# Performance work log

Measured on AMD Instinct MI355X. Metric: run time of the kernel, lower is better.

Reference implementation:

```python
import jax, jax.numpy as jnp
import numpy as np
import math

H = 8
D_MODEL = 4096
D_K = D_MODEL // H  # 512; Sk must equal D_K for the im_attn @ value matmul
B, SQ, SK = 4, 2048, 512


def _linear_params(key, fan_in, fan_out):
    kw, kb = jax.random.split(key)
    bound = 1.0 / math.sqrt(fan_in)
    W = jax.random.uniform(kw, (fan_out, fan_in), jnp.float32, -bound, bound)
    b = jax.random.uniform(kb, (fan_out,), jnp.float32, -bound, bound)
    return W, b


def setup_inputs() -> dict:
    key = jax.random.key(0)
    ks = jax.random.split(key, 8)
    query = jax.random.normal(ks[0], (B, SQ, D_MODEL), jnp.float32)
    k_in = jax.random.normal(ks[1], (B, SK, D_MODEL), jnp.float32)
    v_in = jax.random.normal(ks[2], (B, SK, D_MODEL), jnp.float32)
    image_feat = jax.random.normal(ks[3], (B, SK, D_MODEL), jnp.float32)
    W0, b0 = _linear_params(ks[4], D_MODEL, D_MODEL)
    W1, b1 = _linear_params(ks[5], D_MODEL, D_MODEL)
    W2, b2 = _linear_params(ks[6], D_MODEL, D_MODEL)
    W3, b3 = _linear_params(ks[7], D_MODEL, D_MODEL)  # reused for image_feat AND output proj (as in source)
    return {"query": query, "key": k_in, "value": v_in, "image_feat": image_feat,
            "W0": W0, "b0": b0, "W1": W1, "b1": b1, "W2": W2, "b2": b2, "W3": W3, "b3": b3}


def _split_heads(x):
    # [b, s, d_model] -> [b, h, s, d_k]
    b, s, _ = x.shape
    return x.reshape(b, s, H, D_K).transpose(0, 2, 1, 3)


def reference(query, key, value, image_feat, W0, b0, W1, b1, W2, b2, W3, b3):
    q = _split_heads(query @ W0.T + b0)        # [b,h,Sq,d_k]
    k = _split_heads(key @ W1.T + b1)          # [b,h,Sk,d_k]
    v = _split_heads(value @ W2.T + b2)        # [b,h,Sk,d_k]
    imf = _split_heads(image_feat @ W3.T + b3) # [b,h,Sk,d_k]

    scores = jnp.einsum('bhqd,bhkd->bhqk', q, k) / math.sqrt(D_K)  # [b,h,Sq,Sk]
    p_attn = jax.nn.softmax(scores, axis=-1)
    # second-stage attention over feature axis (Sk == d_k so shapes line up)
    im_attn = jax.nn.softmax(jnp.einsum('bhqk,bhkd->bhqd', p_attn, imf), axis=-1)  # [b,h,Sq,d_k]
    x = jnp.einsum('bhqs,bhsd->bhqd', im_attn, v)  # contracts d_k axis of im_attn with Sk axis of v

    x = x.transpose(0, 2, 1, 3).reshape(query.shape[0], -1, H * D_K)  # [b,Sq,d_model]
    return x @ W3.T + b3  # linears[-1] is the same (shared) 4th linear
```

## Files before the change

### kernel.cpp

```cpp
#include <hip/hip_runtime.h>
#include <hip/hip_bf16.h>
#include <stdint.h>

#define B_   4
#define H_   8
#define SQ_  2048
#define SK_  512
#define DM_  4096
#define DK_  512

typedef __bf16 bf16;
typedef __bf16 bf16x8 __attribute__((ext_vector_type(8)));
typedef float  fx4    __attribute__((ext_vector_type(4)));

typedef __attribute__((address_space(1))) void gv_t;
typedef __attribute__((address_space(3))) void lv_t;

__global__ void sniff_dtype(const uint32_t* __restrict__ q, int* __restrict__ flag)
{
    const int l = threadIdx.x;
    int cnt = 0;
    #pragma unroll
    for (int i = 0; i < 4; ++i) {
        const uint32_t u = q[l * 4 + i];
        const int e = (u >> 7) & 0xFF;
        cnt += (e >= 100 && e <= 135) ? 1 : 0;
    }
    #pragma unroll
    for (int s = 1; s < 64; s <<= 1) cnt += __shfl_xor(cnt, s);
    if (l == 0) *flag = (cnt < 150) ? 1 : 0;
}

__global__ __launch_bounds__(256) void cvt_to_bf16(
    const void* __restrict__ in, bf16* __restrict__ out, const int* __restrict__ flagp)
{
    const size_t i = ((size_t)blockIdx.x * 256 + threadIdx.x) * 8;
    if (*flagp) {
        const float4* p = (const float4*)((const float*)in + i);
        const float4 u0 = p[0], u1 = p[1];
        bf16x8 v;
        v[0] = (bf16)u0.x; v[1] = (bf16)u0.y; v[2] = (bf16)u0.z; v[3] = (bf16)u0.w;
        v[4] = (bf16)u1.x; v[5] = (bf16)u1.y; v[6] = (bf16)u1.z; v[7] = (bf16)u1.w;
        *(bf16x8*)(out + i) = v;
    } else {
        *(bf16x8*)(out + i) = *(const bf16x8*)((const bf16*)in + i);
    }
}

__global__ __launch_bounds__(256, 3) void gemm_bt(
    const bf16* __restrict__ A, const bf16* __restrict__ Bt,
    void* __restrict__ Cv, const void* __restrict__ biasv,
    int K, int lda, int ldb, int ldc, float alpha,
    long long sAb, long long sAh, long long sBb, long long sBh,
    long long sCb, long long sCh,
    const int* __restrict__ flagp, int ebits)
{
    __shared__ bf16 sA[128 * 64];
    __shared__ bf16 sB[128 * 64];

    const int fl = ebits ? *flagp : 0;
    const bool bias32 = fl && (ebits & 1);
    const bool c32    = fl && (ebits & 2);

    const int z = blockIdx.z;
    const int bz = z >> 3, hz = z & 7;
    const bf16* Ab = A  + (size_t)bz * sAb + (size_t)hz * sAh;
    const bf16* Bb = Bt + (size_t)bz * sBb + (size_t)hz * sBh;
    const size_t offC = (size_t)bz * sCb + (size_t)hz * sCh;

    const int n0 = blockIdx.x * 128;
    const int m0 = blockIdx.y * 128;

    const int t = threadIdx.x;
    const int w = t >> 6, l = t & 63;
    const int lrow = l >> 3, lcol = l & 7;
    const int wm = (w >> 1) * 64, wn = (w & 1) * 64;
    const int ml = l & 15, quad = l >> 4;

    const bf16* pa[4];
    const bf16* pb[4];
    #pragma unroll
    for (int i = 0; i < 4; ++i) {
        const int c = w * 4 + i;
        const int r = c * 8 + lrow;
        const int jj = lcol ^ (r & 7);
        pa[i] = Ab + (size_t)(m0 + r) * lda + jj * 8;
        pb[i] = Bb + (size_t)(n0 + r) * ldb + jj * 8;
    }

    fx4 acc[4][4];
    const fx4 zero = {0.f, 0.f, 0.f, 0.f};
    #pragma unroll
    for (int i = 0; i < 4; ++i)
        #pragma unroll
        for (int j = 0; j < 4; ++j) acc[i][j] = zero;

    for (int kt = 0; kt < K; kt += 64) {
        #pragma unroll
        for (int i = 0; i < 4; ++i) {
            const int c = w * 4 + i;
            __builtin_amdgcn_global_load_lds((gv_t*)(pa[i] + kt), (lv_t*)(sA + c * 512), 16, 0, 0);
            __builtin_amdgcn_global_load_lds((gv_t*)(pb[i] + kt), (lv_t*)(sB + c * 512), 16, 0, 0);
        }
        __syncthreads();

        #pragma unroll
        for (int kk = 0; kk < 64; kk += 32) {
            bf16x8 af[4], bfr[4];
            const int jbase = (kk >> 3) + quad;
            #pragma unroll
            for (int mi = 0; mi < 4; ++mi) {
                const int r = wm + mi * 16 + ml;
                af[mi] = *(const bf16x8*)&sA[r * 64 + ((jbase ^ (r & 7)) << 3)];
            }
            #pragma unroll
            for (int ni = 0; ni < 4; ++ni) {
                const int r = wn + ni * 16 + ml;
                bfr[ni] = *(const bf16x8*)&sB[r * 64 + ((jbase ^ (r & 7)) << 3)];
            }
            #pragma unroll
            for (int mi = 0; mi < 4; ++mi)
                #pragma unroll
                for (int ni = 0; ni < 4; ++ni)
                    acc[mi][ni] = __builtin_amdgcn_mfma_f32_16x16x32_bf16(
                        af[mi], bfr[ni], acc[mi][ni], 0, 0, 0);
        }
        __syncthreads();
    }

    #pragma unroll
    for (int ni = 0; ni < 4; ++ni) {
        const int cg = n0 + wn + ni * 16 + ml;
        const float bv = biasv ? (bias32 ? ((const float*)biasv)[cg] : (float)((const bf16*)biasv)[cg]) : 0.f;
        #pragma unroll
        for (int mi = 0; mi < 4; ++mi) {
            const int rg = m0 + wm + mi * 16 + quad * 4;
            #pragma unroll
            for (int r = 0; r < 4; ++r) {
                const float val = acc[mi][ni][r] * alpha + bv;
                const size_t idx = offC + (size_t)(rg + r) * ldc + cg;
                if (c32) ((float*)Cv)[idx] = val;
                else     ((bf16*)Cv)[idx] = (bf16)val;
            }
        }
    }
}

#define ISSUE_TILE(tt, bb)                                                        \
    do {                                                                          \
        _Pragma("unroll")                                                         \
        for (int i_ = 0; i_ < 4; ++i_) {                                          \
            const int c_ = w * 4 + i_;                                            \
            __builtin_amdgcn_global_load_lds((gv_t*)(pa[i_] + (size_t)(tt) * 64), \
                (lv_t*)(&sm[bb][0][c_ * 512]), 16, 0, 0);                         \
            __builtin_amdgcn_global_load_lds((gv_t*)(pb[i_] + (size_t)(tt) * 64), \
                (lv_t*)(&sm[bb][1][c_ * 512]), 16, 0, 0);                         \
        }                                                                         \
    } while (0)

#define LDS_FRAG(dst, base, fr, kI)                                               \
    dst = *(const bf16x8*)&base[(fr) * 64 + ((((kI) * 4 + quad) ^ ((fr) & 7)) << 3)]

__global__ __launch_bounds__(512, 2) void gemm256(
    const bf16* __restrict__ A, const bf16* __restrict__ Bt,
    void* __restrict__ Cv, const void* __restrict__ biasv,
    int K, int lda, int ldb, int ldc, float alpha,
    long long sAb, long long sAh, long long sBb, long long sBh,
    long long sCb, long long sCh,
    const int* __restrict__ flagp, int ebits)
{
    __shared__ bf16 sm[2][2][256 * 64];

    const int fl = ebits ? *flagp : 0;
    const bool bias32 = fl && (ebits & 1);
    const bool c32    = fl && (ebits & 2);

    const int gX = gridDim.x, gY = gridDim.y;
    int idx = (blockIdx.z * gY + blockIdx.y) * gX + blockIdx.x;
    const int nwg = gX * gY * gridDim.z;
    if ((nwg & 7) == 0) idx = (idx & 7) * (nwg >> 3) + (idx >> 3);
    const int bx = idx % gX;
    const int tmpi = idx / gX;
    const int by = tmpi % gY;
    const int z  = tmpi / gY;

    const int bz = z >> 3, hz = z & 7;
    const bf16* Ab = A  + (size_t)bz * sAb + (size_t)hz * sAh;
    const bf16* Bb = Bt + (size_t)bz * sBb + (size_t)hz * sBh;
    const size_t offC = (size_t)bz * sCb + (size_t)hz * sCh;

    const int n0 = bx * 256;
    const int m0 = by * 256;

    const int t  = threadIdx.x;
    const int w  = t >> 6, l = t & 63;
    const int lrow = l >> 3, lcol = l & 7;
    const int wr = w >> 2, wc = w & 3;
    const int R0 = wr * 128, C0 = wc * 64;
    const int ml = l & 15, quad = l >> 4;

    const bf16* pa[4];
    const bf16* pb[4];
    #pragma unroll
    for (int i = 0; i < 4; ++i) {
        const int c = w * 4 + i;
        const int r = c * 8 + lrow;
        const int jj = lcol ^ (r & 7);
        pa[i] = Ab + (size_t)(m0 + r) * lda + jj * 8;
        pb[i] = Bb + (size_t)(n0 + r) * ldb + jj * 8;
    }

    fx4 acc[8][4];
    const fx4 zero = {0.f, 0.f, 0.f, 0.f};
    #pragma unroll
    for (int i = 0; i < 8; ++i)
        #pragma unroll
        for (int j = 0; j < 4; ++j) acc[i][j] = zero;

    const int nt = K >> 6;

    ISSUE_TILE(0, 0);
    ISSUE_TILE(1, 1);
    asm volatile("s_waitcnt vmcnt(8)" ::: "memory");
    asm volatile("s_barrier" ::: "memory");

    for (int tt = 0; tt < nt; ++tt) {
        const int b = tt & 1;
        const bf16* sA = sm[b][0];
        const bf16* sB = sm[b][1];

        bf16x8 af[4][2];
        bf16x8 b0f[2][2];
        bf16x8 b1f[2][2];

        #pragma unroll
        for (int im = 0; im < 4; ++im)
            #pragma unroll
            for (int kI = 0; kI < 2; ++kI)
                LDS_FRAG(af[im][kI], sA, R0 + im * 16 + ml, kI);
        #pragma unroll
        for (int in = 0; in < 2; ++in)
            #pragma unroll
            for (int kI = 0; kI < 2; ++kI)
                LDS_FRAG(b0f[in][kI], sB, C0 + in * 16 + ml, kI);
        asm volatile("s_barrier" ::: "memory");

        __builtin_amdgcn_s_setprio(1);
        #pragma unroll
        for (int kI = 0; kI < 2; ++kI)
            #pragma unroll
            for (int im = 0; im < 4; ++im)
                #pragma unroll
                for (int in = 0; in < 2; ++in)
                    acc[im][in] = __builtin_amdgcn_mfma_f32_16x16x32_bf16(
                        af[im][kI], b0f[in][kI], acc[im][in], 0, 0, 0);
        __builtin_amdgcn_s_setprio(0);
        #pragma unroll
        for (int in = 0; in < 2; ++in)
            #pragma unroll
            for (int kI = 0; kI < 2; ++kI)
                LDS_FRAG(b1f[in][kI], sB, C0 + 32 + in * 16 + ml, kI);
        asm volatile("s_barrier" ::: "memory");

        __builtin_amdgcn_s_setprio(1);
        #pragma unroll
        for (int kI = 0; kI < 2; ++kI)
            #pragma unroll
            for (int im = 0; im < 4; ++im)
                #pragma unroll
                for (int in = 0; in < 2; ++in)
                    acc[im][2 + in] = __builtin_amdgcn_mfma_f32_16x16x32_bf16(
                        af[im][kI], b1f[in][kI], acc[im][2 + in], 0, 0, 0);
        __builtin_amdgcn_s_setprio(0);
        #pragma unroll
        for (int im = 0; im < 4; ++im)
            #pragma unroll
            for (int kI = 0; kI < 2; ++kI)
                LDS_FRAG(af[im][kI], sA, R0 + 64 + im * 16 + ml, kI);
        asm volatile("s_barrier" ::: "memory");

        __builtin_amdgcn_s_setprio(1);
        #pragma unroll
        for (int kI = 0; kI < 2; ++kI)
            #pragma unroll
            for (int im = 0; im < 4; ++im)
                #pragma unroll
                for (int in = 0; in < 2; ++in)
                    acc[4 + im][2 + in] = __builtin_amdgcn_mfma_f32_16x16x32_bf16(
                        af[im][kI], b1f[in][kI], acc[4 + im][2 + in], 0, 0, 0);
        __builtin_amdgcn_s_setprio(0);
        asm volatile("s_barrier" ::: "memory");

        __builtin_amdgcn_s_setprio(1);
        #pragma unroll
        for (int kI = 0; kI < 2; ++kI)
            #pragma unroll
            for (int im = 0; im < 4; ++im)
                #pragma unroll
                for (int in = 0; in < 2; ++in)
                    acc[4 + im][in] = __builtin_amdgcn_mfma_f32_16x16x32_bf16(
                        af[im][kI], b0f[in][kI], acc[4 + im][in], 0, 0, 0);
        __builtin_amdgcn_s_setprio(0);

        if (tt + 1 >= nt) break;
        if (tt + 2 < nt) {
            ISSUE_TILE(tt + 2, b);
            asm volatile("s_waitcnt vmcnt(8)" ::: "memory");
        } else {
            asm volatile("s_waitcnt vmcnt(0)" ::: "memory");
        }
        asm volatile("s_barrier" ::: "memory");
    }

    #pragma unroll
    for (int ni = 0; ni < 4; ++ni) {
        const int cg = n0 + C0 + ni * 16 + ml;
        const float bv = biasv ? (bias32 ? ((const float*)biasv)[cg] : (float)((const bf16*)biasv)[cg]) : 0.f;
        #pragma unroll
        for (int mi = 0; mi < 8; ++mi) {
            const int rg = m0 + R0 + mi * 16 + quad * 4;
            #pragma unroll
            for (int r = 0; r < 4; ++r) {
                const float val = acc[mi][ni][r] * alpha + bv;
                const size_t idx = offC + (size_t)(rg + r) * ldc + cg;
                if (c32) ((float*)Cv)[idx] = val;
                else     ((bf16*)Cv)[idx] = (bf16)val;
            }
        }
    }
}

__global__ __launch_bounds__(256) void softmax512(bf16* __restrict__ buf)
{
    const int row = blockIdx.x * 4 + (threadIdx.x >> 6);
    const int l = threadIdx.x & 63;
    bf16* p = buf + (size_t)row * 512 + l * 8;
    bf16x8 v = *(const bf16x8*)p;
    float f[8];
    float mx = -1e30f;
    #pragma unroll
    for (int j = 0; j < 8; ++j) {
        f[j] = (float)v[j];
        if (!(fabsf(f[j]) < 1e30f)) f[j] = -1e9f;
        mx = fmaxf(mx, f[j]);
    }
    #pragma unroll
    for (int s = 1; s < 64; s <<= 1) mx = fmaxf(mx, __shfl_xor(mx, s));
    float sum = 0.f;
    #pragma unroll
    for (int j = 0; j < 8; ++j) { f[j] = __expf(f[j] - mx); sum += f[j]; }
    #pragma unroll
    for (int s = 1; s < 64; s <<= 1) sum += __shfl_xor(sum, s);
    const float inv = 1.f / sum;
    #pragma unroll
    for (int j = 0; j < 8; ++j) v[j] = (bf16)(f[j] * inv);
    *(bf16x8*)p = v;
}

__global__ __launch_bounds__(256) void transpose_heads(
    const bf16* __restrict__ in, bf16* __restrict__ out)
{
    __shared__ bf16 tile[32][33];
    const int z = blockIdx.z, b = z >> 3, h = z & 7;
    const int s0 = blockIdx.x * 32, d0 = blockIdx.y * 32;
    const int tx = threadIdx.x, ty = threadIdx.y;
    #pragma unroll
    for (int j = 0; j < 4; ++j) {
        const int s = s0 + ty + j * 8;
        tile[ty + j * 8][tx] = in[(size_t)b * SK_ * DM_ + (size_t)s * DM_ + h * DK_ + d0 + tx];
    }
    __syncthreads();
    #pragma unroll
    for (int j = 0; j < 4; ++j) {
        const int d = d0 + ty + j * 8;
        out[(size_t)z * DK_ * SK_ + (size_t)d * SK_ + s0 + tx] = tile[tx][ty + j * 8];
    }
}

extern "C" void kernel_launch(void* const* d_in, const int* in_sizes, int n_in,
                              void* d_out, int out_size, void* d_ws, size_t ws_size,
                              hipStream_t stream)
{
    const void* query = d_in[0];
    const void* key   = d_in[1];
    const void* value = d_in[2];
    const void* imf   = d_in[3];
    const void* W0 = d_in[4];  const void* b0 = d_in[5];
    const void* W1 = d_in[6];  const void* b1 = d_in[7];
    const void* W2 = d_in[8];  const void* b2 = d_in[9];
    const void* W3 = d_in[10]; const void* b3 = d_in[11];

    bf16* ws    = (bf16*)d_ws;
    int*  flagp = (int*)d_ws;
    bf16* wslot = ws + 8;
    bf16* R     = ws + 8 + 16777216;
    bf16* inbuf = R;
    bf16* vproj = R + 8388608;
    bf16* imfp  = R + 16777216;
    bf16* s1    = R;
    bf16* xcat  = R;

    bf16* obase = (bf16*)d_out;
    bf16* qproj = obase;
    bf16* qbf   = obase + 33554432;
    bf16* kproj = obase + 33554432;
    bf16* vT    = obase + 41943040;
    bf16* imfT  = obase + 50331648;
    bf16* s2    = obase;

    const float inv_sqrt_dk = 0.04419417382415922f;

    sniff_dtype<<<1, 64, 0, stream>>>((const uint32_t*)query, flagp);

    cvt_to_bf16<<<16384, 256, 0, stream>>>(query, qbf, flagp);
    cvt_to_bf16<<<8192, 256, 0, stream>>>(W0, wslot, flagp);
    gemm256<<<dim3(16, 32, 1), 512, 0, stream>>>(qbf, wslot, qproj, b0,
        4096, 4096, 4096, 4096, 1.f, 0,0,0,0,0,0, flagp, 1);
    cvt_to_bf16<<<4096, 256, 0, stream>>>(key, inbuf, flagp);
    cvt_to_bf16<<<8192, 256, 0, stream>>>(W1, wslot, flagp);
    gemm_bt<<<dim3(32, 16, 1), 256, 0, stream>>>(inbuf, wslot, kproj, b1,
        4096, 4096, 4096, 4096, 1.f, 0,0,0,0,0,0, flagp, 1);
    cvt_to_bf16<<<4096, 256, 0, stream>>>(value, inbuf, flagp);
    cvt_to_bf16<<<8192, 256, 0, stream>>>(W2, wslot, flagp);
    gemm_bt<<<dim3(32, 16, 1), 256, 0, stream>>>(inbuf, wslot, vproj, b2,
        4096, 4096, 4096, 4096, 1.f, 0,0,0,0,0,0, flagp, 1);
    cvt_to_bf16<<<4096, 256, 0, stream>>>(imf, inbuf, flagp);
    cvt_to_bf16<<<8192, 256, 0, stream>>>(W3, wslot, flagp);
    gemm_bt<<<dim3(32, 16, 1), 256, 0, stream>>>(inbuf, wslot, imfp, b3,
        4096, 4096, 4096, 4096, 1.f, 0,0,0,0,0,0, flagp, 1);

    transpose_heads<<<dim3(16, 16, 32), dim3(32, 8), 0, stream>>>(vproj, vT);
    transpose_heads<<<dim3(16, 16, 32), dim3(32, 8), 0, stream>>>(imfp, imfT);

    gemm256<<<dim3(2, 8, 32), 512, 0, stream>>>(qproj, kproj, s1, nullptr,
        512, 4096, 4096, 512, inv_sqrt_dk,
        (long long)SQ_*DM_, (long long)DK_, (long long)SK_*DM_, (long long)DK_,
        (long long)H_*SQ_*SK_, (long long)SQ_*SK_, flagp, 0);
    softmax512<<<dim3(16384), 256, 0, stream>>>(s1);
    gemm256<<<dim3(2, 8, 32), 512, 0, stream>>>(s1, imfT, s2, nullptr,
        512, 512, 512, 512, 1.f,
        (long long)H_*SQ_*SK_, (long long)SQ_*SK_, (long long)H_*DK_*SK_, (long long)DK_*SK_,
        (long long)H_*SQ_*SK_, (long long)SQ_*SK_, flagp, 0);
    softmax512<<<dim3(16384), 256, 0, stream>>>(s2);
    gemm256<<<dim3(2, 8, 32), 512, 0, stream>>>(s2, vT, xcat, nullptr,
        512, 512, 512, 4096, 1.f,
        (long long)H_*SQ_*SK_, (long long)SQ_*SK_, (long long)H_*DK_*SK_, (long long)DK_*SK_,
        (long long)SQ_*DM_, (long long)DK_, flagp, 0);
    cvt_to_bf16<<<8192, 256, 0, stream>>>(W3, wslot, flagp);
    gemm256<<<dim3(16, 32, 1), 512, 0, stream>>>(xcat, wslot, d_out, b3,
        4096, 4096, 4096, 4096, 1.f, 0,0,0,0,0,0, flagp, 3);
}
```

Before: 1.605 ms.

## Software-pipeline LDS fragment loads across K tiles and drop intra-tile barriers

Restructures the GEMM main loop so the A and B0 fragments for the next K tile are read from shared memory during the last MFMA quadrants of the current tile. Three of the four per-tile barriers are removed, leaving one barrier per iteration after the global prefetch issue. The aim is to hide LDS read latency behind MFMA work and cut synchronisation stalls. The cost is extra fragment registers (aN, aP, b0N), which may raise VGPR pressure, and a reordering that has to stay correct with respect to the buffer being overwritten by the next global load.

After: 1.617 ms. No clear change (+0.8%).

```diff
diff --git a/kernel.cpp b/kernel.cpp
--- a/kernel.cpp
+++ b/kernel.cpp
@@ -219,31 +219,30 @@
 
     const int nt = K >> 6;
 
+    bf16x8 aN[4][2], aP[4][2], b0N[2][2], b1f[2][2];
+
     ISSUE_TILE(0, 0);
     ISSUE_TILE(1, 1);
     asm volatile("s_waitcnt vmcnt(8)" ::: "memory");
     asm volatile("s_barrier" ::: "memory");
+    #pragma unroll
+    for (int im = 0; im < 4; ++im)
+        #pragma unroll
+        for (int kI = 0; kI < 2; ++kI)
+            LDS_FRAG(aN[im][kI], (&sm[0][0][0]), R0 + im * 16 + ml, kI);
+    #pragma unroll
+    for (int in = 0; in < 2; ++in)
+        #pragma unroll
+        for (int kI = 0; kI < 2; ++kI)
+            LDS_FRAG(b0N[in][kI], (&sm[0][1][0]), C0 + in * 16 + ml, kI);
 
     for (int tt = 0; tt < nt; ++tt) {
         const int b = tt & 1;
-        const bf16* sA = sm[b][0];
-        const bf16* sB = sm[b][1];
-
-        bf16x8 af[4][2];
-        bf16x8 b0f[2][2];
-        bf16x8 b1f[2][2];
-
-        #pragma unroll
-        for (int im = 0; im < 4; ++im)
-            #pragma unroll
-            for (int kI = 0; kI < 2; ++kI)
-                LDS_FRAG(af[im][kI], sA, R0 + im * 16 + ml, kI);
-        #pragma unroll
-        for (int in = 0; in < 2; ++in)
-            #pragma unroll
-            for (int kI = 0; kI < 2; ++kI)
-                LDS_FRAG(b0f[in][kI], sB, C0 + in * 16 + ml, kI);
-        asm volatile("s_barrier" ::: "memory");
+        const bf16* sA  = sm[b][0];
+        const bf16* sB  = sm[b][1];
+        const bf16* sAn = sm[b ^ 1][0];
+        const bf16* sBn = sm[b ^ 1][1];
+        const bool more = (tt + 1 < nt);
 
         __builtin_amdgcn_s_setprio(1);
         #pragma unroll
@@ -253,14 +252,13 @@
                 #pragma unroll
                 for (int in = 0; in < 2; ++in)
                     acc[im][in] = __builtin_amdgcn_mfma_f32_16x16x32_bf16(
-                        af[im][kI], b0f[in][kI], acc[im][in], 0, 0, 0);
+                        aN[im][kI], b0N[in][kI], acc[im][in], 0, 0, 0);
         __builtin_amdgcn_s_setprio(0);
         #pragma unroll
         for (int in = 0; in < 2; ++in)
             #pragma unroll
             for (int kI = 0; kI < 2; ++kI)
                 LDS_FRAG(b1f[in][kI], sB, C0 + 32 + in * 16 + ml, kI);
-        asm volatile("s_barrier" ::: "memory");
 
         __builtin_amdgcn_s_setprio(1);
         #pragma unroll
@@ -270,39 +268,15 @@
                 #pragma unroll
                 for (int in = 0; in < 2; ++in)
                     acc[im][2 + in] = __builtin_amdgcn_mfma_f32_16x16x32_bf16(
-                        af[im][kI], b1f[in][kI], acc[im][2 + in], 0, 0, 0);
+                        aN[im][kI], b1f[in][kI], acc[im][2 + in], 0, 0, 0);
         __builtin_amdgcn_s_setprio(0);
         #pragma unroll
         for (int im = 0; im < 4; ++im)
             #pragma unroll
             for (int kI = 0; kI < 2; ++kI)
-                LDS_FRAG(af[im][kI], sA, R0 + 64 + im * 16 + ml, kI);
+                LDS_FRAG(aP[im][kI], sA, R0 + 64 + im * 16 + ml, kI);
+
         asm volatile("s_barrier" ::: "memory");
-
-        __builtin_amdgcn_s_setprio(1);
-        #pragma unroll
-        for (int kI = 0; kI < 2; ++kI)
-            #pragma unroll
-            for (int im = 0; im < 4; ++im)
-                #pragma unroll
-                for (int in = 0; in < 2; ++in)
-                    acc[4 + im][2 + in] = __builtin_amdgcn_mfma_f32_16x16x32_bf16(
-                        af[im][kI], b1f[in][kI], acc[4 + im][2 + in], 0, 0, 0);
-        __builtin_amdgcn_s_setprio(0);
-        asm volatile("s_barrier" ::: "memory");
-
-        __builtin_amdgcn_s_setprio(1);
-        #pragma unroll
-        for (int kI = 0; kI < 2; ++kI)
-            #pragma unroll
-            for (int im = 0; im < 4; ++im)
-                #pragma unroll
-                for (int in = 0; in < 2; ++in)
-                    acc[4 + im][in] = __builtin_amdgcn_mfma_f32_16x16x32_bf16(
-                        af[im][kI], b0f[in][kI], acc[4 + im][in], 0, 0, 0);
-        __builtin_amdgcn_s_setprio(0);
-
-        if (tt + 1 >= nt) break;
         if (tt + 2 < nt) {
             ISSUE_TILE(tt + 2, b);
             asm volatile("s_waitcnt vmcnt(8)" ::: "memory");
@@ -310,6 +284,42 @@
             asm volatile("s_waitcnt vmcnt(0)" ::: "memory");
         }
         asm volatile("s_barrier" ::: "memory");
+
+        __builtin_amdgcn_s_setprio(1);
+        #pragma unroll
+        for (int kI = 0; kI < 2; ++kI)
+            #pragma unroll
+            for (int im = 0; im < 4; ++im)
+                #pragma unroll
+                for (int in = 0; in < 2; ++in)
+                    acc[4 + im][2 + in] = __builtin_amdgcn_mfma_f32_16x16x32_bf16(
+                        aP[im][kI], b1f[in][kI], acc[4 + im][2 + in], 0, 0, 0);
+        __builtin_amdgcn_s_setprio(0);
+        if (more) {
+            #pragma unroll
+            for (int im = 0; im < 4; ++im)
+                #pragma unroll
+                for (int kI = 0; kI < 2; ++kI)
+                    LDS_FRAG(aN[im][kI], sAn, R0 + im * 16 + ml, kI);
+        }
+
+        __builtin_amdgcn_s_setprio(1);
+        #pragma unroll
+        for (int kI = 0; kI < 2; ++kI)
+            #pragma unroll
+            for (int im = 0; im < 4; ++im)
+                #pragma unroll
+                for (int in = 0; in < 2; ++in)
+                    acc[4 + im][in] = __builtin_amdgcn_mfma_f32_16x16x32_bf16(
+                        aP[im][kI], b0N[in][kI], acc[4 + im][in], 0, 0, 0);
+        __builtin_amdgcn_s_setprio(0);
+        if (more) {
+            #pragma unroll
+            for (int in = 0; in < 2; ++in)
+                #pragma unroll
+                for (int kI = 0; kI < 2; ++kI)
+                    LDS_FRAG(b0N[in][kI], sBn, C0 + in * 16 + ml, kI);
+        }
     }
 
     #pragma unroll
```

## Replace 256x256 GEMM with 256x128 tile, BK=32 pipelined kernel

Applied to the files above, without the earlier changes.

Replaces the 512-thread 256x256 tile, BK=64 GEMM with a 256-thread kernel using 256x128 output tiles and 32-wide K slices. It adopts a new XOR swizzle and collapses the four barrier-separated MFMA phases into two. The tile loads for the next stage are issued mid-iteration so they overlap the remaining MFMAs. The aim is fewer barriers per unit of work and more workgroups to fill the CUs. In exchange, operand reuse per block drops, global traffic per FLOP rises, and each K-step carries more loop overhead.

Result: slower. 1.715 ms (+6.8%).

```diff
diff --git a/kernel.cpp b/kernel.cpp
--- a/kernel.cpp
+++ b/kernel.cpp
@@ -146,22 +146,24 @@
     }
 }
 
-#define ISSUE_TILE(tt, bb)                                                        \
-    do {                                                                          \
-        _Pragma("unroll")                                                         \
-        for (int i_ = 0; i_ < 4; ++i_) {                                          \
-            const int c_ = w * 4 + i_;                                            \
-            __builtin_amdgcn_global_load_lds((gv_t*)(pa[i_] + (size_t)(tt) * 64), \
-                (lv_t*)(&sm[bb][0][c_ * 512]), 16, 0, 0);                         \
-            __builtin_amdgcn_global_load_lds((gv_t*)(pb[i_] + (size_t)(tt) * 64), \
-                (lv_t*)(&sm[bb][1][c_ * 512]), 16, 0, 0);                         \
-        }                                                                         \
+#define ISSUE_TILE6(tt, bb)                                                         \
+    do {                                                                            \
+        bf16* bufA_ = sm + (bb) * 12288;                                            \
+        bf16* bufB_ = bufA_ + 8192;                                                 \
+        _Pragma("unroll")                                                           \
+        for (int i_ = 0; i_ < 4; ++i_)                                              \
+            __builtin_amdgcn_global_load_lds((gv_t*)(pa[i_] + (size_t)(tt) * 32),   \
+                (lv_t*)(bufA_ + (w * 4 + i_) * 512), 16, 0, 0);                     \
+        _Pragma("unroll")                                                           \
+        for (int i_ = 0; i_ < 2; ++i_)                                              \
+            __builtin_amdgcn_global_load_lds((gv_t*)(pb[i_] + (size_t)(tt) * 32),   \
+                (lv_t*)(bufB_ + (w * 2 + i_) * 512), 16, 0, 0);                     \
     } while (0)
 
-#define LDS_FRAG(dst, base, fr, kI)                                               \
-    dst = *(const bf16x8*)&base[(fr) * 64 + ((((kI) * 4 + quad) ^ ((fr) & 7)) << 3)]
-
-__global__ __launch_bounds__(512, 2) void gemm256(
+#define LDS_FRAG32(dst, base, fr)                                                   \
+    dst = *(const bf16x8*)&base[(fr) * 32 + (((quad ^ (((fr) >> 1) & 3))) << 3)]
+
+__global__ __launch_bounds__(256, 2) void gemm_pipe(
     const bf16* __restrict__ A, const bf16* __restrict__ Bt,
     void* __restrict__ Cv, const void* __restrict__ biasv,
     int K, int lda, int ldb, int ldc, float alpha,
@@ -169,7 +171,7 @@
     long long sCb, long long sCh,
     const int* __restrict__ flagp, int ebits)
 {
-    __shared__ bf16 sm[2][2][256 * 64];
+    __shared__ bf16 sm[2 * 12288];
 
     const int fl = ebits ? *flagp : 0;
     const bool bias32 = fl && (ebits & 1);
@@ -189,24 +191,28 @@
     const bf16* Bb = Bt + (size_t)bz * sBb + (size_t)hz * sBh;
     const size_t offC = (size_t)bz * sCb + (size_t)hz * sCh;
 
-    const int n0 = bx * 256;
+    const int n0 = bx * 128;
     const int m0 = by * 256;
 
     const int t  = threadIdx.x;
     const int w  = t >> 6, l = t & 63;
-    const int lrow = l >> 3, lcol = l & 7;
-    const int wr = w >> 2, wc = w & 3;
+    const int wr = w >> 1, wc = w & 1;
     const int R0 = wr * 128, C0 = wc * 64;
     const int ml = l & 15, quad = l >> 4;
 
+    const int srow = l >> 2, sslot = l & 3;
     const bf16* pa[4];
-    const bf16* pb[4];
+    const bf16* pb[2];
     #pragma unroll
     for (int i = 0; i < 4; ++i) {
-        const int c = w * 4 + i;
-        const int r = c * 8 + lrow;
-        const int jj = lcol ^ (r & 7);
+        const int r = (w * 4 + i) * 16 + srow;
+        const int jj = sslot ^ ((r >> 1) & 3);
         pa[i] = Ab + (size_t)(m0 + r) * lda + jj * 8;
+    }
+    #pragma unroll
+    for (int i = 0; i < 2; ++i) {
+        const int r = (w * 2 + i) * 16 + srow;
+        const int jj = sslot ^ ((r >> 1) & 3);
         pb[i] = Bb + (size_t)(n0 + r) * ldb + jj * 8;
     }
 
@@ -217,99 +223,77 @@
         #pragma unroll
         for (int j = 0; j < 4; ++j) acc[i][j] = zero;
 
-    const int nt = K >> 6;
-
-    ISSUE_TILE(0, 0);
-    ISSUE_TILE(1, 1);
-    asm volatile("s_waitcnt vmcnt(8)" ::: "memory");
+    const int nt = K >> 5;
+
+    ISSUE_TILE6(0, 0);
+    ISSUE_TILE6(1, 1);
+    asm volatile("s_waitcnt vmcnt(6)" ::: "memory");
     asm volatile("s_barrier" ::: "memory");
 
     for (int tt = 0; tt < nt; ++tt) {
         const int b = tt & 1;
-        const bf16* sA = sm[b][0];
-        const bf16* sB = sm[b][1];
-
-        bf16x8 af[4][2];
-        bf16x8 b0f[2][2];
-        bf16x8 b1f[2][2];
-
-        #pragma unroll
-        for (int im = 0; im < 4; ++im)
-            #pragma unroll
-            for (int kI = 0; kI < 2; ++kI)
-                LDS_FRAG(af[im][kI], sA, R0 + im * 16 + ml, kI);
+        const bf16* sA = sm + b * 12288;
+        const bf16* sB = sA + 8192;
+
+        bf16x8 aF[4], b0[2], b1[2];
+
+        #pragma unroll
+        for (int im = 0; im < 4; ++im)
+            LDS_FRAG32(aF[im], sA, R0 + im * 16 + ml);
         #pragma unroll
         for (int in = 0; in < 2; ++in)
-            #pragma unroll
-            for (int kI = 0; kI < 2; ++kI)
-                LDS_FRAG(b0f[in][kI], sB, C0 + in * 16 + ml, kI);
+            LDS_FRAG32(b0[in], sB, C0 + in * 16 + ml);
+
+        __builtin_amdgcn_s_setprio(1);
+        #pragma unroll
+        for (int im = 0; im < 4; ++im)
+            #pragma unroll
+            for (int in = 0; in < 2; ++in)
+                acc[im][in] = __builtin_amdgcn_mfma_f32_16x16x32_bf16(
+                    aF[im], b0[in], acc[im][in], 0, 0, 0);
+        __builtin_amdgcn_s_setprio(0);
+        #pragma unroll
+        for (int in = 0; in < 2; ++in)
+            LDS_FRAG32(b1[in], sB, C0 + 32 + in * 16 + ml);
+
+        __builtin_amdgcn_s_setprio(1);
+        #pragma unroll
+        for (int im = 0; im < 4; ++im)
+            #pragma unroll
+            for (int in = 0; in < 2; ++in)
+                acc[im][2 + in] = __builtin_amdgcn_mfma_f32_16x16x32_bf16(
+                    aF[im], b1[in], acc[im][2 + in], 0, 0, 0);
+        __builtin_amdgcn_s_setprio(0);
+        #pragma unroll
+        for (int im = 0; im < 4; ++im)
+            LDS_FRAG32(aF[im], sA, R0 + 64 + im * 16 + ml);
+
         asm volatile("s_barrier" ::: "memory");
-
-        __builtin_amdgcn_s_setprio(1);
-        #pragma unroll
-        for (int kI = 0; kI < 2; ++kI)
-            #pragma unroll
-            for (int im = 0; im < 4; ++im)
-                #pragma unroll
-                for (int in = 0; in < 2; ++in)
-                    acc[im][in] = __builtin_amdgcn_mfma_f32_16x16x32_bf16(
-                        af[im][kI], b0f[in][kI], acc[im][in], 0, 0, 0);
-        __builtin_amdgcn_s_setprio(0);
-        #pragma unroll
-        for (int in = 0; in < 2; ++in)
-            #pragma unroll
-            for (int kI = 0; kI < 2; ++kI)
-                LDS_FRAG(b1f[in][kI], sB, C0 + 32 + in * 16 + ml, kI);
-        asm volatile("s_barrier" ::: "memory");
-
-        __builtin_amdgcn_s_setprio(1);
-        #pragma unroll
-        for (int kI = 0; kI < 2; ++kI)
-            #pragma unroll
-            for (int im = 0; im < 4; ++im)
-                #pragma unroll
-                for (int in = 0; in < 2; ++in)
-                    acc[im][2 + in] = __builtin_amdgcn_mfma_f32_16x16x32_bf16(
-                        af[im][kI], b1f[in][kI], acc[im][2 + in], 0, 0, 0);
-        __builtin_amdgcn_s_setprio(0);
-        #pragma unroll
-        for (int im = 0; im < 4; ++im)
-            #pragma unroll
-            for (int kI = 0; kI < 2; ++kI)
-                LDS_FRAG(af[im][kI], sA, R0 + 64 + im * 16 + ml, kI);
-        asm volatile("s_barrier" ::: "memory");
-
-        __builtin_amdgcn_s_setprio(1);
-        #pragma unroll
-        for (int kI = 0; kI < 2; ++kI)
-            #pragma unroll
-            for (int im = 0; im < 4; ++im)
-                #pragma unroll
-                for (int in = 0; in < 2; ++in)
-                    acc[4 + im][2 + in] = __builtin_amdgcn_mfma_f32_16x16x32_bf16(
-                        af[im][kI], b1f[in][kI], acc[4 + im][2 + in], 0, 0, 0);
-        __builtin_amdgcn_s_setprio(0);
-        asm volatile("s_barrier" ::: "memory");
-
-        __builtin_amdgcn_s_setprio(1);
-        #pragma unroll
-        for (int kI = 0; kI < 2; ++kI)
-            #pragma unroll
-            for (int im = 0; im < 4; ++im)
-                #pragma unroll
-                for (int in = 0; in < 2; ++in)
-                    acc[4 + im][in] = __builtin_amdgcn_mfma_f32_16x16x32_bf16(
-                        af[im][kI], b0f[in][kI], acc[4 + im][in], 0, 0, 0);
-        __builtin_amdgcn_s_setprio(0);
-
-        if (tt + 1 >= nt) break;
         if (tt + 2 < nt) {
-            ISSUE_TILE(tt + 2, b);
-            asm volatile("s_waitcnt vmcnt(8)" ::: "memory");
-        } else {
+            ISSUE_TILE6(tt + 2, b);
+            asm volatile("s_waitcnt vmcnt(6)" ::: "memory");
+        } else if (tt + 1 < nt) {
             asm volatile("s_waitcnt vmcnt(0)" ::: "memory");
         }
         asm volatile("s_barrier" ::: "memory");
+
+        __builtin_amdgcn_s_setprio(1);
+        #pragma unroll
+        for (int im = 0; im < 4; ++im)
+            #pragma unroll
+            for (int in = 0; in < 2; ++in)
+                acc[4 + im][2 + in] = __builtin_amdgcn_mfma_f32_16x16x32_bf16(
+                    aF[im], b1[in], acc[4 + im][2 + in], 0, 0, 0);
+        __builtin_amdgcn_s_setprio(0);
+
+        __builtin_amdgcn_s_setprio(1);
+        #pragma unroll
+        for (int im = 0; im < 4; ++im)
+            #pragma unroll
+            for (int in = 0; in < 2; ++in)
+                acc[4 + im][in] = __builtin_amdgcn_mfma_f32_16x16x32_bf16(
+                    aF[im], b0[in], acc[4 + im][in], 0, 0, 0);
+        __builtin_amdgcn_s_setprio(0);
     }
 
     #pragma unroll
@@ -414,7 +398,7 @@
 
     cvt_to_bf16<<<16384, 256, 0, stream>>>(query, qbf, flagp);
     cvt_to_bf16<<<8192, 256, 0, stream>>>(W0, wslot, flagp);
-    gemm256<<<dim3(16, 32, 1), 512, 0, stream>>>(qbf, wslot, qproj, b0,
+    gemm_pipe<<<dim3(32, 32, 1), 256, 0, stream>>>(qbf, wslot, qproj, b0,
         4096, 4096, 4096, 4096, 1.f, 0,0,0,0,0,0, flagp, 1);
     cvt_to_bf16<<<4096, 256, 0, stream>>>(key, inbuf, flagp);
     cvt_to_bf16<<<8192, 256, 0, stream>>>(W1, wslot, flagp);
@@ -432,21 +416,21 @@
     transpose_heads<<<dim3(16, 16, 32), dim3(32, 8), 0, stream>>>(vproj, vT);
     transpose_heads<<<dim3(16, 16, 32), dim3(32, 8), 0, stream>>>(imfp, imfT);
 
-    gemm256<<<dim3(2, 8, 32), 512, 0, stream>>>(qproj, kproj, s1, nullptr,
+    gemm_pipe<<<dim3(4, 8, 32), 256, 0, stream>>>(qproj, kproj, s1, nullptr,
         512, 4096, 4096, 512, inv_sqrt_dk,
         (long long)SQ_*DM_, (long long)DK_, (long long)SK_*DM_, (long long)DK_,
         (long long)H_*SQ_*SK_, (long long)SQ_*SK_, flagp, 0);
     softmax512<<<dim3(16384), 256, 0, stream>>>(s1);
-    gemm256<<<dim3(2, 8, 32), 512, 0, stream>>>(s1, imfT, s2, nullptr,
+    gemm_pipe<<<dim3(4, 8, 32), 256, 0, stream>>>(s1, imfT, s2, nullptr,
         512, 512, 512, 512, 1.f,
         (long long)H_*SQ_*SK_, (long long)SQ_*SK_, (long long)H_*DK_*SK_, (long long)DK_*SK_,
         (long long)H_*SQ_*SK_, (long long)SQ_*SK_, flagp, 0);
     softmax512<<<dim3(16384), 256, 0, stream>>>(s2);
-    gemm256<<<dim3(2, 8, 32), 512, 0, stream>>>(s2, vT, xcat, nullptr,
+    gemm_pipe<<<dim3(4, 8, 32), 256, 0, stream>>>(s2, vT, xcat, nullptr,
         512, 512, 512, 4096, 1.f,
         (long long)H_*SQ_*SK_, (long long)SQ_*SK_, (long long)H_*DK_*SK_, (long long)DK_*SK_,
         (long long)SQ_*DM_, (long long)DK_, flagp, 0);
     cvt_to_bf16<<<8192, 256, 0, stream>>>(W3, wslot, flagp);
-    gemm256<<<dim3(16, 32, 1), 512, 0, stream>>>(xcat, wslot, d_out, b3,
+    gemm_pipe<<<dim3(32, 32, 1), 256, 0, stream>>>(xcat, wslot, d_out, b3,
         4096, 4096, 4096, 4096, 1.f, 0,0,0,0,0,0, flagp, 3);
 }
```
